# Kernel tuning notes

Hardware: AMD Instinct MI355X
Metric: run time of the kernel (lower is better)

The kernel has to match this reference:

```python
import jax, jax.numpy as jnp
import numpy as np

N_HEADS = 4
D_HEAD = 64
SCALE = D_HEAD ** -0.5


def setup_inputs() -> dict:
    key = jax.random.key(0)
    k0, k1, k2, k3, k4 = jax.random.split(key, 5)
    C = 256
    return {
        "x": jax.random.normal(k0, (32, C, 32, 32), dtype=jnp.float32),
        "W_qkv": jax.random.normal(k1, (C, 3 * N_HEADS * D_HEAD), dtype=jnp.float32) * 0.02,
        "b_qkv": jax.random.normal(k2, (3 * N_HEADS * D_HEAD,), dtype=jnp.float32) * 0.02,
        "W_out": jax.random.normal(k3, (C, C), dtype=jnp.float32) * 0.02,
        "b_out": jax.random.normal(k4, (C,), dtype=jnp.float32) * 0.02,
    }


def reference(x, W_qkv, b_qkv, W_out, b_out):
    b, c, h, w = x.shape
    # [B, C, H, W] -> [B, S, C], S = H*W  (NOTE: GroupNorm is defined in the
    # original module but never applied in forward; we match that exactly.)
    xs = x.reshape(b, c, h * w).transpose(0, 2, 1)
    qkv = (xs @ W_qkv + b_qkv).reshape(b, -1, N_HEADS, 3 * D_HEAD)
    q, k, v = jnp.split(qkv, 3, axis=-1)  # each [B, S, H, D]
    scores = jnp.einsum('bihd,bjhd->bijh', q, k) * SCALE  # [B, S, S, H]
    attn = jax.nn.softmax(scores, axis=2)  # softmax over key index j
    res = jnp.einsum('bijh,bjhd->bihd', attn, v).reshape(b, -1, N_HEADS * D_HEAD)
    res = res @ W_out + b_out + xs
    return res.transpose(0, 2, 1).reshape(b, c, h, w)
```

## Files before the change

### kernel.cpp

```cpp
#include <hip/hip_runtime.h>

#define NH 4
#define DH 64
#define SS 1024
#define CC 256
#define BB 32

typedef __attribute__((ext_vector_type(8))) short short8;
typedef __attribute__((ext_vector_type(4))) float floatx4;

#define MFMA16(a, b, c) __builtin_amdgcn_mfma_f32_16x16x32_bf16(a, b, c, 0, 0, 0)

#define QSCALE 0.18033688011112042f

__device__ __forceinline__ short f2bf(float f) {
    union { float f; unsigned u; } v; v.f = f;
    unsigned r = (v.u + 0x7fffu + ((v.u >> 16) & 1u)) >> 16;
    return (short)r;
}
__device__ __forceinline__ unsigned bfrn(float f) {
    union { float f; unsigned u; } v; v.f = f;
    return (v.u + 0x7fffu + ((v.u >> 16) & 1u)) >> 16;
}
__device__ __forceinline__ unsigned pk2_trunc(float a, float b) {
    union { float f; unsigned u; } ua, ub; ua.f = a; ub.f = b;
    return (ua.u >> 16) | (ub.u & 0xFFFF0000u);
}
__device__ __forceinline__ unsigned pk2_rn(float a, float b) {
    return bfrn(a) | (bfrn(b) << 16);
}

__global__ __launch_bounds__(256) void k_prep(const float* __restrict__ x,
                                              const float* __restrict__ Wqkv,
                                              const float* __restrict__ Wout,
                                              short* __restrict__ xs,
                                              short* __restrict__ Wqkv_t,
                                              short* __restrict__ Wout_t) {
    int bid = blockIdx.x;
    if (bid < 2048) {
        __shared__ float tile[64][65];
        int b = bid >> 6;
        int s0 = ((bid >> 2) & 15) * 64;
        int c0 = (bid & 3) * 64;
        int t = threadIdx.x;
        int tx = t & 63, ty = t >> 6;
        for (int i = 0; i < 16; ++i) {
            int c = ty + i * 4;
            tile[tx][c] = x[((b * CC) + (c0 + c)) * SS + s0 + tx];
        }
        __syncthreads();
        for (int i = 0; i < 8; ++i) {
            int s = (t >> 5) + i * 8;
            int cp = (t & 31) * 2;
            short2 v;
            v.x = f2bf(tile[s][cp]);
            v.y = f2bf(tile[s][cp + 1]);
            *(short2*)(&xs[((b * SS) + (s0 + s)) * CC + c0 + cp]) = v;
        }
    } else {
        int idx = (bid - 2048) * 256 + threadIdx.x;
        if (idx < 768 * 256) {
            int n = idx >> 8, k = idx & 255;
            Wqkv_t[idx] = f2bf(Wqkv[k * 768 + n]);
        } else {
            int j = idx - 768 * 256;
            int c = j >> 8, k = j & 255;
            Wout_t[j] = f2bf(Wout[k * 256 + c]);
        }
    }
}

__global__ __launch_bounds__(256) void k_qkv(const short* __restrict__ xs,
                                             const short* __restrict__ Wt,
                                             const float* __restrict__ bqkv,
                                             short* __restrict__ qw,
                                             short* __restrict__ kw,
                                             short* __restrict__ vtw) {
    __shared__ short smem[10240];
    short* As = smem;
    short* Bs = smem + 5120;
    int m0 = blockIdx.x * 128;
    int n0 = blockIdx.y * 128;
    int t = threadIdx.x;
    int lane = t & 63, wid = t >> 6;
    int wr = wid >> 1, wc = wid & 1;
    int c16 = lane & 15, qd = lane >> 4;

    floatx4 acc[4][4] = {};
    short8 pa[2], pb[2];

    {
        for (int j = 0; j < 2; ++j) {
            int id = j * 256 + t, row = id >> 2, cc = id & 3;
            pa[j] = *(const short8*)(&xs[(m0 + row) * CC + cc * 8]);
            pb[j] = *(const short8*)(&Wt[(n0 + row) * CC + cc * 8]);
        }
    }
    for (int kt = 0; kt < 8; ++kt) {
        if (kt) __syncthreads();
        for (int j = 0; j < 2; ++j) {
            int id = j * 256 + t, row = id >> 2, cc = id & 3;
            *(short8*)(&As[row * 40 + cc * 8]) = pa[j];
            *(short8*)(&Bs[row * 40 + cc * 8]) = pb[j];
        }
        __syncthreads();
        if (kt < 7) {
            for (int j = 0; j < 2; ++j) {
                int id = j * 256 + t, row = id >> 2, cc = id & 3;
                pa[j] = *(const short8*)(&xs[(m0 + row) * CC + (kt + 1) * 32 + cc * 8]);
                pb[j] = *(const short8*)(&Wt[(n0 + row) * CC + (kt + 1) * 32 + cc * 8]);
            }
        }
        short8 av[4], bv[4];
        for (int i = 0; i < 4; ++i) {
            av[i] = *(const short8*)(&As[(wr * 64 + i * 16 + c16) * 40 + qd * 8]);
            bv[i] = *(const short8*)(&Bs[(wc * 64 + i * 16 + c16) * 40 + qd * 8]);
        }
        for (int mi = 0; mi < 4; ++mi)
            for (int ni = 0; ni < 4; ++ni)
                acc[mi][ni] = MFMA16(av[mi], bv[ni], acc[mi][ni]);
    }

    int b = m0 >> 10, sbase = m0 & 1023;
    float bias4[4];
    for (int ni = 0; ni < 4; ++ni)
        bias4[ni] = bqkv[n0 + wc * 64 + ni * 16 + c16];

    for (int half = 0; half < 2; ++half) {
        int seg = (n0 >> 6) + half;
        int sel = seg % 3, h = seg / 3;
        int bh = b * NH + h;
        __syncthreads();
        if (wc == half) {
            if (sel == 2) {
                for (int mi = 0; mi < 4; ++mi)
                    for (int ni = 0; ni < 4; ++ni)
                        for (int r = 0; r < 4; ++r)
                            smem[(ni * 16 + c16) * 136 + wr * 64 + mi * 16 + qd * 4 + r] =
                                f2bf(acc[mi][ni][r] + bias4[ni]);
            } else {
                float sc = (sel == 0) ? QSCALE : 1.f;
                for (int mi = 0; mi < 4; ++mi)
                    for (int ni = 0; ni < 4; ++ni)
                        for (int r = 0; r < 4; ++r)
                            smem[(wr * 64 + mi * 16 + qd * 4 + r) * 80 + ni * 16 + c16] =
                                f2bf((acc[mi][ni][r] + bias4[ni]) * sc);
            }
        }
        __syncthreads();
        if (sel == 2) {
            for (int i = 0; i < 4; ++i) {
                int d = (t >> 4) + i * 16;
                int sc8 = (t & 15) * 8;
                *(short8*)(&vtw[(bh * DH + d) * SS + sbase + sc8]) =
                    *(const short8*)(&smem[d * 136 + sc8]);
            }
        } else {
            short* dst = (sel == 0) ? qw : kw;
            for (int i = 0; i < 4; ++i) {
                int srow = (t >> 3) + i * 32;
                int d8 = (t & 7) * 8;
                *(short8*)(&dst[(bh * SS + sbase + srow) * DH + d8]) =
                    *(const short8*)(&smem[srow * 80 + d8]);
            }
        }
    }
}

__global__ __launch_bounds__(256) void k_attn(const short* __restrict__ qw,
                                              const short* __restrict__ kw,
                                              const short* __restrict__ vtw,
                                              short* __restrict__ res) {
    __shared__ __align__(16) short Ks[64 * 72];
    __shared__ __align__(16) short Vts[64 * 72];
    __shared__ __align__(16) short Pt[4 * 16 * 76];
    int bid = blockIdx.x;
    int q0 = (bid >> 7) * 128;
    int bh = bid & 127;
    int t = threadIdx.x;
    int lane = t & 63, w = t >> 6;
    int c16 = lane & 15, qd = lane >> 4;
    const short* qp = qw + bh * SS * DH;
    const short* kp = kw + bh * SS * DH;
    const short* vp = vtw + bh * DH * SS;

    short8 qfrag[2][2];
    for (int g = 0; g < 2; ++g)
        for (int ks = 0; ks < 2; ++ks)
            qfrag[g][ks] = *(const short8*)(
                &qp[(q0 + g * 64 + w * 16 + c16) * DH + ks * 32 + qd * 8]);

    float l_i[2] = {};
    floatx4 o_acc[2][4] = {};

    short8 kreg[2], vreg[2];
    for (int j = 0; j < 2; ++j) {
        int id = j * 256 + t, row = id >> 3, cc = id & 7;
        kreg[j] = *(const short8*)(&kp[row * DH + cc * 8]);
        vreg[j] = *(const short8*)(&vp[row * SS + cc * 8]);
    }

    int pbase = w * 16 * 76;
    for (int kt = 0; kt < 16; ++kt) {
        if (kt) __syncthreads();
        for (int j = 0; j < 2; ++j) {
            int id = j * 256 + t, row = id >> 3, cc = id & 7;
            *(short8*)(&Ks[row * 72 + cc * 8]) = kreg[j];
            *(short8*)(&Vts[row * 72 + cc * 8]) = vreg[j];
        }
        __syncthreads();
        if (kt < 15) {
            for (int j = 0; j < 2; ++j) {
                int id = j * 256 + t, row = id >> 3, cc = id & 7;
                kreg[j] = *(const short8*)(&kp[((kt + 1) * 64 + row) * DH + cc * 8]);
                vreg[j] = *(const short8*)(&vp[row * SS + (kt + 1) * 64 + cc * 8]);
            }
        }

        short8 kf[2][4], vf[2][4];
        for (int ks = 0; ks < 2; ++ks)
            for (int ji = 0; ji < 4; ++ji) {
                kf[ks][ji] = *(const short8*)(&Ks[(ji * 16 + c16) * 72 + ks * 32 + qd * 8]);
                vf[ks][ji] = *(const short8*)(&Vts[(ji * 16 + c16) * 72 + ks * 32 + qd * 8]);
            }

        for (int g = 0; g < 2; ++g) {
            floatx4 sacc[4] = {};
            for (int ks = 0; ks < 2; ++ks)
                for (int ji = 0; ji < 4; ++ji)
                    sacc[ji] = MFMA16(kf[ks][ji], qfrag[g][ks], sacc[ji]);

            for (int ji = 0; ji < 4; ++ji) {
                float e0 = __builtin_amdgcn_exp2f(sacc[ji][0]);
                float e1 = __builtin_amdgcn_exp2f(sacc[ji][1]);
                float e2 = __builtin_amdgcn_exp2f(sacc[ji][2]);
                float e3 = __builtin_amdgcn_exp2f(sacc[ji][3]);
                l_i[g] += (e0 + e1) + (e2 + e3);
                uint2 pw;
                pw.x = pk2_trunc(e0, e1);
                pw.y = pk2_trunc(e2, e3);
                *(uint2*)(&Pt[pbase + c16 * 76 + ji * 16 + qd * 4]) = pw;
            }

            for (int ks2 = 0; ks2 < 2; ++ks2) {
                short8 pf = *(const short8*)(&Pt[pbase + c16 * 76 + ks2 * 32 + qd * 8]);
                for (int di = 0; di < 4; ++di)
                    o_acc[g][di] = MFMA16(vf[ks2][di], pf, o_acc[g][di]);
            }
        }
    }

    for (int g = 0; g < 2; ++g) {
        float l = l_i[g];
        l += __shfl_xor(l, 16);
        l += __shfl_xor(l, 32);
        l_i[g] = 1.f / l;
    }

    int b = bh >> 2, h = bh & 3;
    for (int g = 0; g < 2; ++g) {
        int s = q0 + g * 64 + w * 16 + c16;
        long base = (long)(b * SS + s) * CC + h * DH;
        float inv = l_i[g];
        for (int di = 0; di < 4; ++di) {
            uint2 ow;
            ow.x = pk2_rn(o_acc[g][di][0] * inv, o_acc[g][di][1] * inv);
            ow.y = pk2_rn(o_acc[g][di][2] * inv, o_acc[g][di][3] * inv);
            *(uint2*)(&res[base + di * 16 + qd * 4]) = ow;
        }
    }
}

__global__ __launch_bounds__(256) void k_out(const short* __restrict__ res,
                                             const short* __restrict__ Wot,
                                             const float* __restrict__ bout,
                                             const float* __restrict__ x,
                                             float* __restrict__ out) {
    __shared__ short As[128 * 40];
    __shared__ short Bs[128 * 40];
    int b = blockIdx.z;
    int m0 = blockIdx.y * 128;
    int n0 = blockIdx.x * 128;
    int t = threadIdx.x;
    int lane = t & 63, wid = t >> 6;
    int wr = wid >> 1, wc = wid & 1;
    int c16 = lane & 15, qd = lane >> 4;

    floatx4 acc[4][4] = {};
    short8 pa[2], pbv[2];
    for (int j = 0; j < 2; ++j) {
        int id = j * 256 + t, row = id >> 2, cc = id & 3;
        pa[j] = *(const short8*)(&Wot[(m0 + row) * CC + cc * 8]);
        pbv[j] = *(const short8*)(&res[(b * SS + n0 + row) * CC + cc * 8]);
    }

    for (int kt = 0; kt < 8; ++kt) {
        if (kt) __syncthreads();
        for (int j = 0; j < 2; ++j) {
            int id = j * 256 + t, row = id >> 2, cc = id & 3;
            *(short8*)(&As[row * 40 + cc * 8]) = pa[j];
            *(short8*)(&Bs[row * 40 + cc * 8]) = pbv[j];
        }
        __syncthreads();
        if (kt < 7) {
            for (int j = 0; j < 2; ++j) {
                int id = j * 256 + t, row = id >> 2, cc = id & 3;
                pa[j] = *(const short8*)(&Wot[(m0 + row) * CC + (kt + 1) * 32 + cc * 8]);
                pbv[j] = *(const short8*)(&res[(b * SS + n0 + row) * CC + (kt + 1) * 32 + cc * 8]);
            }
        }
        short8 av[4], bv[4];
        for (int i = 0; i < 4; ++i) {
            av[i] = *(const short8*)(&As[(wr * 64 + i * 16 + c16) * 40 + qd * 8]);
            bv[i] = *(const short8*)(&Bs[(wc * 64 + i * 16 + c16) * 40 + qd * 8]);
        }
        for (int mi = 0; mi < 4; ++mi)
            for (int ni = 0; ni < 4; ++ni)
                acc[mi][ni] = MFMA16(av[mi], bv[ni], acc[mi][ni]);
    }

    for (int mi = 0; mi < 4; ++mi) {
        for (int r = 0; r < 4; ++r) {
            int c = m0 + wr * 64 + mi * 16 + qd * 4 + r;
            float bias = bout[c];
            for (int ni = 0; ni < 4; ++ni) {
                int s = n0 + wc * 64 + ni * 16 + c16;
                float v = acc[mi][ni][r] + bias + x[((b * CC) + c) * SS + s];
                out[((b * CC) + c) * SS + s] = v;
            }
        }
    }
}

extern "C" void kernel_launch(void* const* d_in, const int* in_sizes, int n_in,
                              void* d_out, int out_size, void* d_ws, size_t ws_size,
                              hipStream_t stream) {
    const float* x    = (const float*)d_in[0];
    const float* Wqkv = (const float*)d_in[1];
    const float* bqkv = (const float*)d_in[2];
    const float* Wout = (const float*)d_in[3];
    const float* bout = (const float*)d_in[4];
    float* out = (float*)d_out;

    char* ws = (char*)d_ws;
    short* xs_res = (short*)(ws);
    short* qw     = (short*)(ws + 16777216);
    short* kw     = (short*)(ws + 33554432);
    short* vtw    = (short*)(ws + 50331648);
    short* Wqkv_t = (short*)(ws + 67108864);
    short* Wout_t = (short*)(ws + 67502080);

    k_prep<<<dim3(3072), 256, 0, stream>>>(x, Wqkv, Wout, xs_res, Wqkv_t, Wout_t);
    k_qkv<<<dim3(256, 6), 256, 0, stream>>>(xs_res, Wqkv_t, bqkv, qw, kw, vtw);
    k_attn<<<dim3(1024), 256, 0, stream>>>(qw, kw, vtw, xs_res);
    k_out<<<dim3(8, 2, 32), 256, 0, stream>>>(xs_res, Wout_t, bout, x, out);
}
```

Before: 184.4 us.

## Load attention K/V fragments straight from global memory and swizzle QKV block order

```diff
diff --git a/kernel.cpp b/kernel.cpp
--- a/kernel.cpp
+++ b/kernel.cpp
@@ -79,8 +79,10 @@
     __shared__ short smem[10240];
     short* As = smem;
     short* Bs = smem + 5120;
-    int m0 = blockIdx.x * 128;
-    int n0 = blockIdx.y * 128;
+    int bid = blockIdx.x;
+    int idx = bid >> 3;
+    int m0 = ((bid & 7) * 32 + idx / 6) * 128;
+    int n0 = (idx % 6) * 128;
     int t = threadIdx.x;
     int lane = t & 63, wid = t >> 6;
     int wr = wid >> 1, wc = wid & 1;
@@ -171,9 +173,7 @@
                                               const short* __restrict__ kw,
                                               const short* __restrict__ vtw,
                                               short* __restrict__ res) {
-    __shared__ __align__(16) short Ks[64 * 72];
-    __shared__ __align__(16) short Vts[64 * 72];
-    __shared__ __align__(16) short Pt[4 * 16 * 76];
+    __shared__ __align__(16) short Pt[4 * 2 * 16 * 76];
     int bid = blockIdx.x;
     int q0 = (bid >> 7) * 128;
     int bh = bid & 127;
@@ -181,8 +181,8 @@
     int lane = t & 63, w = t >> 6;
     int c16 = lane & 15, qd = lane >> 4;
     const short* qp = qw + bh * SS * DH;
-    const short* kp = kw + bh * SS * DH;
-    const short* vp = vtw + bh * DH * SS;
+    const short* kpl = kw + (size_t)bh * SS * DH + c16 * DH + qd * 8;
+    const short* vpl = vtw + (size_t)bh * DH * SS + (size_t)c16 * SS + qd * 8;
 
     short8 qfrag[2][2];
     for (int g = 0; g < 2; ++g)
@@ -193,38 +193,17 @@
     float l_i[2] = {};
     floatx4 o_acc[2][4] = {};
 
-    short8 kreg[2], vreg[2];
-    for (int j = 0; j < 2; ++j) {
-        int id = j * 256 + t, row = id >> 3, cc = id & 7;
-        kreg[j] = *(const short8*)(&kp[row * DH + cc * 8]);
-        vreg[j] = *(const short8*)(&vp[row * SS + cc * 8]);
-    }
-
-    int pbase = w * 16 * 76;
+    int pb0 = w * 2 * 16 * 76;
     for (int kt = 0; kt < 16; ++kt) {
-        if (kt) __syncthreads();
-        for (int j = 0; j < 2; ++j) {
-            int id = j * 256 + t, row = id >> 3, cc = id & 7;
-            *(short8*)(&Ks[row * 72 + cc * 8]) = kreg[j];
-            *(short8*)(&Vts[row * 72 + cc * 8]) = vreg[j];
-        }
-        __syncthreads();
-        if (kt < 15) {
-            for (int j = 0; j < 2; ++j) {
-                int id = j * 256 + t, row = id >> 3, cc = id & 7;
-                kreg[j] = *(const short8*)(&kp[((kt + 1) * 64 + row) * DH + cc * 8]);
-                vreg[j] = *(const short8*)(&vp[row * SS + (kt + 1) * 64 + cc * 8]);
-            }
-        }
-
         short8 kf[2][4], vf[2][4];
-        for (int ks = 0; ks < 2; ++ks)
-            for (int ji = 0; ji < 4; ++ji) {
-                kf[ks][ji] = *(const short8*)(&Ks[(ji * 16 + c16) * 72 + ks * 32 + qd * 8]);
-                vf[ks][ji] = *(const short8*)(&Vts[(ji * 16 + c16) * 72 + ks * 32 + qd * 8]);
+        for (int ji = 0; ji < 4; ++ji)
+            for (int ks = 0; ks < 2; ++ks) {
+                kf[ks][ji] = *(const short8*)(kpl + (kt * 64 + ji * 16) * DH + ks * 32);
+                vf[ks][ji] = *(const short8*)(vpl + (size_t)(ji * 16) * SS + kt * 64 + ks * 32);
             }
 
         for (int g = 0; g < 2; ++g) {
+            int pbase = pb0 + g * 16 * 76;
             floatx4 sacc[4] = {};
             for (int ks = 0; ks < 2; ++ks)
                 for (int ji = 0; ji < 4; ++ji)
@@ -351,7 +330,7 @@
     short* Wout_t = (short*)(ws + 67502080);
 
     k_prep<<<dim3(3072), 256, 0, stream>>>(x, Wqkv, Wout, xs_res, Wqkv_t, Wout_t);
-    k_qkv<<<dim3(256, 6), 256, 0, stream>>>(xs_res, Wqkv_t, bqkv, qw, kw, vtw);
+    k_qkv<<<dim3(1536), 256, 0, stream>>>(xs_res, Wqkv_t, bqkv, qw, kw, vtw);
     k_attn<<<dim3(1024), 256, 0, stream>>>(qw, kw, vtw, xs_res);
     k_out<<<dim3(8, 2, 32), 256, 0, stream>>>(xs_res, Wout_t, bout, x, out);
 }
```

Measured after the change: 254.5 us. 38.0% more time.

## Enlarge attention query tile, store Q transposed, and remap QKV block order

Applied to the files above, without the earlier changes.

```diff
diff --git a/kernel.cpp b/kernel.cpp
--- a/kernel.cpp
+++ b/kernel.cpp
@@ -73,14 +73,16 @@
 __global__ __launch_bounds__(256) void k_qkv(const short* __restrict__ xs,
                                              const short* __restrict__ Wt,
                                              const float* __restrict__ bqkv,
-                                             short* __restrict__ qw,
+                                             short* __restrict__ qtw,
                                              short* __restrict__ kw,
                                              short* __restrict__ vtw) {
     __shared__ short smem[10240];
     short* As = smem;
     short* Bs = smem + 5120;
-    int m0 = blockIdx.x * 128;
-    int n0 = blockIdx.y * 128;
+    int bid = blockIdx.x;
+    int idx = bid >> 3;
+    int m0 = ((bid & 7) * 32 + idx / 6) * 128;
+    int n0 = (idx % 6) * 128;
     int t = threadIdx.x;
     int lane = t & 63, wid = t >> 6;
     int wr = wid >> 1, wc = wid & 1;
@@ -89,12 +91,10 @@
     floatx4 acc[4][4] = {};
     short8 pa[2], pb[2];
 
-    {
-        for (int j = 0; j < 2; ++j) {
-            int id = j * 256 + t, row = id >> 2, cc = id & 3;
-            pa[j] = *(const short8*)(&xs[(m0 + row) * CC + cc * 8]);
-            pb[j] = *(const short8*)(&Wt[(n0 + row) * CC + cc * 8]);
-        }
+    for (int j = 0; j < 2; ++j) {
+        int id = j * 256 + t, row = id >> 2, cc = id & 3;
+        pa[j] = *(const short8*)(&xs[(m0 + row) * CC + cc * 8]);
+        pb[j] = *(const short8*)(&Wt[(n0 + row) * CC + cc * 8]);
     }
     for (int kt = 0; kt < 8; ++kt) {
         if (kt) __syncthreads();
@@ -122,76 +122,82 @@
     }
 
     int b = m0 >> 10, sbase = m0 & 1023;
+    int seg = (n0 >> 6) + wc;
+    int sel = seg % 3, h = seg / 3;
+    int bh = b * NH + h;
     float bias4[4];
     for (int ni = 0; ni < 4; ++ni)
         bias4[ni] = bqkv[n0 + wc * 64 + ni * 16 + c16];
 
-    for (int half = 0; half < 2; ++half) {
-        int seg = (n0 >> 6) + half;
-        int sel = seg % 3, h = seg / 3;
-        int bh = b * NH + h;
-        __syncthreads();
-        if (wc == half) {
-            if (sel == 2) {
-                for (int mi = 0; mi < 4; ++mi)
-                    for (int ni = 0; ni < 4; ++ni)
-                        for (int r = 0; r < 4; ++r)
-                            smem[(ni * 16 + c16) * 136 + wr * 64 + mi * 16 + qd * 4 + r] =
-                                f2bf(acc[mi][ni][r] + bias4[ni]);
-            } else {
-                float sc = (sel == 0) ? QSCALE : 1.f;
-                for (int mi = 0; mi < 4; ++mi)
-                    for (int ni = 0; ni < 4; ++ni)
-                        for (int r = 0; r < 4; ++r)
-                            smem[(wr * 64 + mi * 16 + qd * 4 + r) * 80 + ni * 16 + c16] =
-                                f2bf((acc[mi][ni][r] + bias4[ni]) * sc);
-            }
-        }
-        __syncthreads();
-        if (sel == 2) {
-            for (int i = 0; i < 4; ++i) {
-                int d = (t >> 4) + i * 16;
-                int sc8 = (t & 15) * 8;
-                *(short8*)(&vtw[(bh * DH + d) * SS + sbase + sc8]) =
-                    *(const short8*)(&smem[d * 136 + sc8]);
-            }
-        } else {
-            short* dst = (sel == 0) ? qw : kw;
-            for (int i = 0; i < 4; ++i) {
-                int srow = (t >> 3) + i * 32;
-                int d8 = (t & 7) * 8;
-                *(short8*)(&dst[(bh * SS + sbase + srow) * DH + d8]) =
-                    *(const short8*)(&smem[srow * 80 + d8]);
-            }
-        }
-    }
-}
-
-__global__ __launch_bounds__(256) void k_attn(const short* __restrict__ qw,
-                                              const short* __restrict__ kw,
-                                              const short* __restrict__ vtw,
-                                              short* __restrict__ res) {
+    if (sel != 1) {
+        float sc = (sel == 0) ? QSCALE : 1.f;
+        short* dst = (sel == 0) ? qtw : vtw;
+        for (int ni = 0; ni < 4; ++ni) {
+            int d = ni * 16 + c16;
+            for (int mi = 0; mi < 4; ++mi) {
+                int s = sbase + wr * 64 + mi * 16 + qd * 4;
+                uint2 ow;
+                ow.x = pk2_rn((acc[mi][ni][0] + bias4[ni]) * sc,
+                              (acc[mi][ni][1] + bias4[ni]) * sc);
+                ow.y = pk2_rn((acc[mi][ni][2] + bias4[ni]) * sc,
+                              (acc[mi][ni][3] + bias4[ni]) * sc);
+                *(uint2*)(&dst[(size_t)(bh * DH + d) * SS + s]) = ow;
+            }
+        }
+    }
+
+    int seg0 = n0 >> 6;
+    int kseg = (seg0 % 3 == 1) ? seg0 : (((seg0 + 1) % 3 == 1) ? seg0 + 1 : -1);
+    if (kseg >= 0) {
+        short* Kt = smem;
+        __syncthreads();
+        if (seg == kseg) {
+            for (int mi = 0; mi < 4; ++mi)
+                for (int ni = 0; ni < 4; ++ni)
+                    for (int r = 0; r < 4; ++r)
+                        Kt[(wr * 64 + mi * 16 + qd * 4 + r) * 72 + ni * 16 + c16] =
+                            f2bf(acc[mi][ni][r] + bias4[ni]);
+        }
+        __syncthreads();
+        int bhk = b * NH + kseg / 3;
+        int srow = t >> 1, dh = (t & 1) * 32;
+        short* gdst = &kw[(size_t)(bhk * SS + sbase + srow) * DH + dh];
+        const short* lsrc = &Kt[srow * 72 + dh];
+        for (int k = 0; k < 4; ++k)
+            *(short8*)(gdst + k * 8) = *(const short8*)(lsrc + k * 8);
+    }
+}
+
+__global__ __launch_bounds__(256, 2) void k_attn(const short* __restrict__ qtw,
+                                                 const short* __restrict__ kw,
+                                                 const short* __restrict__ vtw,
+                                                 short* __restrict__ res) {
     __shared__ __align__(16) short Ks[64 * 72];
     __shared__ __align__(16) short Vts[64 * 72];
     __shared__ __align__(16) short Pt[4 * 16 * 76];
     int bid = blockIdx.x;
-    int q0 = (bid >> 7) * 128;
+    int q0 = (bid >> 7) * 256;
     int bh = bid & 127;
     int t = threadIdx.x;
     int lane = t & 63, w = t >> 6;
     int c16 = lane & 15, qd = lane >> 4;
-    const short* qp = qw + bh * SS * DH;
-    const short* kp = kw + bh * SS * DH;
-    const short* vp = vtw + bh * DH * SS;
-
-    short8 qfrag[2][2];
-    for (int g = 0; g < 2; ++g)
-        for (int ks = 0; ks < 2; ++ks)
-            qfrag[g][ks] = *(const short8*)(
-                &qp[(q0 + g * 64 + w * 16 + c16) * DH + ks * 32 + qd * 8]);
-
-    float l_i[2] = {};
-    floatx4 o_acc[2][4] = {};
+    const short* qp = qtw + (size_t)bh * DH * SS;
+    const short* kp = kw + (size_t)bh * SS * DH;
+    const short* vp = vtw + (size_t)bh * DH * SS;
+
+    short8 qfrag[4][2];
+    for (int g = 0; g < 4; ++g) {
+        int s = q0 + g * 64 + w * 16 + c16;
+        for (int ks = 0; ks < 2; ++ks) {
+            short8 q;
+            for (int j = 0; j < 8; ++j)
+                q[j] = qp[(size_t)(ks * 32 + qd * 8 + j) * SS + s];
+            qfrag[g][ks] = q;
+        }
+    }
+
+    float l_i[4] = {};
+    floatx4 o_acc[4][4] = {};
 
     short8 kreg[2], vreg[2];
     for (int j = 0; j < 2; ++j) {
@@ -224,7 +230,7 @@
                 vf[ks][ji] = *(const short8*)(&Vts[(ji * 16 + c16) * 72 + ks * 32 + qd * 8]);
             }
 
-        for (int g = 0; g < 2; ++g) {
+        for (int g = 0; g < 4; ++g) {
             floatx4 sacc[4] = {};
             for (int ks = 0; ks < 2; ++ks)
                 for (int ji = 0; ji < 4; ++ji)
@@ -250,7 +256,7 @@
         }
     }
 
-    for (int g = 0; g < 2; ++g) {
+    for (int g = 0; g < 4; ++g) {
         float l = l_i[g];
         l += __shfl_xor(l, 16);
         l += __shfl_xor(l, 32);
@@ -258,7 +264,7 @@
     }
 
     int b = bh >> 2, h = bh & 3;
-    for (int g = 0; g < 2; ++g) {
+    for (int g = 0; g < 4; ++g) {
         int s = q0 + g * 64 + w * 16 + c16;
         long base = (long)(b * SS + s) * CC + h * DH;
         float inv = l_i[g];
@@ -344,14 +350,14 @@
 
     char* ws = (char*)d_ws;
     short* xs_res = (short*)(ws);
-    short* qw     = (short*)(ws + 16777216);
+    short* qtw    = (short*)(ws + 16777216);
     short* kw     = (short*)(ws + 33554432);
     short* vtw    = (short*)(ws + 50331648);
     short* Wqkv_t = (short*)(ws + 67108864);
     short* Wout_t = (short*)(ws + 67502080);
 
     k_prep<<<dim3(3072), 256, 0, stream>>>(x, Wqkv, Wout, xs_res, Wqkv_t, Wout_t);
-    k_qkv<<<dim3(256, 6), 256, 0, stream>>>(xs_res, Wqkv_t, bqkv, qw, kw, vtw);
-    k_attn<<<dim3(1024), 256, 0, stream>>>(qw, kw, vtw, xs_res);
+    k_qkv<<<dim3(1536), 256, 0, stream>>>(xs_res, Wqkv_t, bqkv, qtw, kw, vtw);
+    k_attn<<<dim3(512), 256, 0, stream>>>(qtw, kw, vtw, xs_res);
     k_out<<<dim3(8, 2, 32), 256, 0, stream>>>(xs_res, Wout_t, bout, x, out);
 }
```

After: 177.5 us. 3.8% less time.
